# Kernel tuning notes

Measured on AMD Instinct MI355X. Metric: run time of the kernel, lower is better.

Reference implementation:

```python
import jax, jax.numpy as jnp
import numpy as np

D_MODEL = 512; D_INNER = 1024; D_STATE = 16; DT_RANK = 32; D_CONV = 4
N_LAYERS = 2; LSPP = 7; N_ROI = 2048; HIDDEN = 4096


def layer_norm(x, g, b, eps=1e-5):
    mu = x.mean(-1, keepdims=True)
    v = ((x - mu) ** 2).mean(-1, keepdims=True)
    return (x - mu) * jax.lax.rsqrt(v + eps) * g + b


def causal_dwconv(u, w, b):
    # u: [N,L,Di], w: [Di,K] depthwise, causal left-pad K-1
    x = jnp.transpose(u, (0, 2, 1))
    out = jax.lax.conv_general_dilated(x, w[:, None, :], (1,), [(D_CONV - 1, 0)],
                                       dimension_numbers=('NCH', 'OIH', 'NCH'),
                                       feature_group_count=D_INNER)
    return jnp.transpose(out, (0, 2, 1)) + b


def selective_scan(u, dt, A, B, C):
    # u, dt: [N,L,Di]; B, C: [N,L,S]; A: [Di,S]
    def step(h, xs):
        dt_t, B_t, C_t, u_t = xs
        dA = jnp.exp(dt_t[..., None] * A)                      # [N,Di,S]
        h = dA * h + (dt_t * u_t)[..., None] * B_t[:, None, :]
        return h, jnp.einsum('nds,ns->nd', h, C_t)
    h0 = jnp.zeros((u.shape[0], D_INNER, D_STATE), u.dtype)
    xs = (jnp.moveaxis(dt, 1, 0), jnp.moveaxis(B, 1, 0),
          jnp.moveaxis(C, 1, 0), jnp.moveaxis(u, 1, 0))
    _, ys = jax.lax.scan(step, h0, xs)
    return jnp.moveaxis(ys, 0, 1)                              # [N,L,Di]


def mamba_block(h, inw, cw, cb, xpw, dtw, dtb, Alog, Dp, ow):
    # decomposed bidirectional mamba ('dbm'): shared in_proj/gate, fwd+bwd scans summed
    xz = h @ inw.T                                             # [N,L,2*Di]
    xi, z = jnp.split(xz, 2, axis=-1)
    ys = []
    for d in range(2):
        u = xi if d == 0 else jnp.flip(xi, axis=1)
        u = jax.nn.silu(causal_dwconv(u, cw[d], cb[d]))
        dbl = u @ xpw[d].T                                     # [N,L,DT_RANK+2S]
        dtr = dbl[..., :DT_RANK]
        B = dbl[..., DT_RANK:DT_RANK + D_STATE]
        C = dbl[..., DT_RANK + D_STATE:]
        dt = jax.nn.softplus(dtr @ dtw[d].T + dtb[d])
        A = -jnp.exp(Alog[d])
        yd = selective_scan(u, dt, A, B, C) + u * Dp[d]
        ys.append(yd if d == 0 else jnp.flip(yd, axis=1))
    return ((ys[0] + ys[1]) * jax.nn.silu(z)) @ ow.T


def setup_inputs() -> dict:
    key = jax.random.key(0)
    ks = iter(jax.random.split(key, 40))
    rn = lambda shape, scale: jax.random.normal(next(ks), shape, dtype=jnp.float32) * scale
    inp = {}
    inp['x_flat'] = rn((N_ROI, D_MODEL * LSPP), 1.0)
    inp['conv_a_w'] = rn((256, 512, 3), (512 * 3) ** -0.5)
    inp['conv_p_w'] = rn((256, 512, 1), 512 ** -0.5)
    inp['se_w1'] = rn((32, 512), 512 ** -0.5)
    inp['se_b1'] = jnp.zeros((32,), jnp.float32)
    inp['se_w2'] = rn((512, 32), 32 ** -0.5)
    inp['se_b2'] = jnp.zeros((512,), jnp.float32)
    inp['ln_g'] = jnp.ones((N_LAYERS, D_MODEL), jnp.float32)
    inp['ln_b'] = jnp.zeros((N_LAYERS, D_MODEL), jnp.float32)
    inp['in_proj_w'] = rn((N_LAYERS, 2 * D_INNER, D_MODEL), D_MODEL ** -0.5)
    inp['conv_w'] = rn((N_LAYERS, 2, D_INNER, D_CONV), D_CONV ** -0.5)
    inp['conv_b'] = jnp.zeros((N_LAYERS, 2, D_INNER), jnp.float32)
    inp['x_proj_w'] = rn((N_LAYERS, 2, DT_RANK + 2 * D_STATE, D_INNER), D_INNER ** -0.5)
    inp['dt_proj_w'] = rn((N_LAYERS, 2, D_INNER, DT_RANK), DT_RANK ** -0.5)
    inp['dt_proj_b'] = rn((N_LAYERS, 2, D_INNER), 0.1) - 4.0
    inp['A_log'] = jnp.log(jnp.arange(1., D_STATE + 1., dtype=jnp.float32)) * jnp.ones((N_LAYERS, 2, D_INNER, D_STATE), jnp.float32)
    inp['D_param'] = jnp.ones((N_LAYERS, 2, D_INNER), jnp.float32)
    inp['out_proj_w'] = rn((N_LAYERS, D_MODEL, D_INNER), D_INNER ** -0.5)
    inp['out_ln_g'] = jnp.ones((D_MODEL,), jnp.float32)
    inp['out_ln_b'] = jnp.zeros((D_MODEL,), jnp.float32)
    inp['mlp_w1'] = rn((HIDDEN, D_MODEL), D_MODEL ** -0.5)
    inp['mlp_b1'] = jnp.zeros((HIDDEN,), jnp.float32)
    inp['mlp_w2'] = rn((HIDDEN, HIDDEN), HIDDEN ** -0.5)
    inp['mlp_b2'] = jnp.zeros((HIDDEN,), jnp.float32)
    return inp


def reference(x_flat, conv_a_w, conv_p_w, se_w1, se_b1, se_w2, se_b2, ln_g, ln_b,
              in_proj_w, conv_w, conv_b, x_proj_w, dt_proj_w, dt_proj_b, A_log,
              D_param, out_proj_w, out_ln_g, out_ln_b, mlp_w1, mlp_b1, mlp_w2, mlp_b2):
    N = x_flat.shape[0]
    x = x_flat.reshape(N, D_MODEL, LSPP)                       # [N,512,7]
    dn = ('NCH', 'OIH', 'NCH')
    # TSSE: strided conv branch + maxpool branch, concat, SE gating; L: 7 -> 4
    a = jax.nn.relu(jax.lax.conv_general_dilated(x, conv_a_w, (2,), [(1, 1)], dimension_numbers=dn))
    p = jax.lax.reduce_window(x, -jnp.inf, jax.lax.max, (1, 1, 3), (1, 1, 2), ((0, 0), (0, 0), (1, 1)))
    p = jax.nn.relu(jax.lax.conv_general_dilated(p, conv_p_w, (1,), [(0, 0)], dimension_numbers=dn))
    y = jnp.concatenate([a, p], axis=1)                        # [N,512,4]
    s = jax.nn.sigmoid(jax.nn.relu(y.mean(-1) @ se_w1.T + se_b1) @ se_w2.T + se_b2)
    y = y * s[:, :, None]
    # Mamba backbone: 2 pre-norm residual DBM blocks (mask is all-ones -> no-op)
    h = jnp.transpose(y, (0, 2, 1))                            # [N,L,512]
    for l in range(N_LAYERS):
        h = h + mamba_block(layer_norm(h, ln_g[l], ln_b[l]), in_proj_w[l], conv_w[l],
                            conv_b[l], x_proj_w[l], dt_proj_w[l], dt_proj_b[l],
                            A_log[l], D_param[l], out_proj_w[l])
    h = layer_norm(h, out_ln_g, out_ln_b)
    feat = h.mean(1)                                           # mean pool over time
    z1 = jax.nn.relu(feat @ mlp_w1.T + mlp_b1)
    return jax.nn.relu(z1 @ mlp_w2.T + mlp_b2)                 # [N,4096]
```

## Files before the change

### kernel.cpp

```cpp
#include <hip/hip_runtime.h>
#include <hip/hip_bf16.h>

typedef __hip_bfloat16 bf16;
typedef __attribute__((ext_vector_type(8))) short s16x8;
typedef __attribute__((ext_vector_type(4))) float f32x4;

__device__ __forceinline__ float u2f(unsigned short u){
  union { unsigned int i; float f; } v; v.i = ((unsigned int)u) << 16; return v.f;
}
__device__ __forceinline__ float bfu(bf16 x){ return __bfloat162float(x); }
__device__ __forceinline__ bf16  f2b(float x){ return __float2bfloat16(x); }

__device__ __forceinline__ void gload16(const void* g, void* l){
  __builtin_amdgcn_global_load_lds(
      (const __attribute__((address_space(1))) void*)g,
      (__attribute__((address_space(3))) void*)l, 16, 0, 0);
}

__device__ __forceinline__ float block_sum256(float v, float* red){
  #pragma unroll
  for (int o = 32; o > 0; o >>= 1) v += __shfl_down(v, o, 64);
  int lane = threadIdx.x & 63, wid = threadIdx.x >> 6;
  if (lane == 0) red[wid] = v;
  __syncthreads();
  float r = red[0] + red[1] + red[2] + red[3];
  __syncthreads();
  return r;
}

__global__ __launch_bounds__(256) void f2b4_kernel(
    const float4* __restrict__ in, ushort4* __restrict__ out, int n4)
{
  int stride = gridDim.x * 256;
  for (int i = blockIdx.x*256 + threadIdx.x; i < n4; i += stride){
    float4 v = in[i];
    ushort4 o;
    o.x = __bfloat16_as_ushort(f2b(v.x));
    o.y = __bfloat16_as_ushort(f2b(v.y));
    o.z = __bfloat16_as_ushort(f2b(v.z));
    o.w = __bfloat16_as_ushort(f2b(v.w));
    out[i] = o;
  }
}

__global__ __launch_bounds__(256) void xpw_pad_kernel(
    const float* __restrict__ xpw, bf16* __restrict__ out)
{
  int idx = blockIdx.x*256 + threadIdx.x;
  if (idx >= 524288) return;
  int l = idx >> 18, rem = idx & 262143, row = rem >> 10, c = rem & 1023;
  int d = row >> 7, r = row & 127;
  float v = (r < 64) ? xpw[(((size_t)l*2 + d)*64 + r)*1024 + c] : 0.f;
  out[idx] = f2b(v);
}

__global__ __launch_bounds__(256) void wdt_pad_kernel(
    const float* __restrict__ dtw, bf16* __restrict__ out)
{
  int idx = blockIdx.x*256 + threadIdx.x;
  if (idx >= 262144) return;
  int ld = idx >> 16, rem = idx & 65535, r = rem >> 6, c = rem & 63;
  float v = (c < 32) ? dtw[((size_t)ld*1024 + r)*32 + c] : 0.f;
  out[idx] = f2b(v);
}

__global__ __launch_bounds__(256) void atab_kernel(
    const float* __restrict__ Alog, float* __restrict__ Atab)
{
  int i = blockIdx.x*256 + threadIdx.x;
  if (i < 65536) Atab[i] = -__expf(Alog[i]);
}

template<int ACT, int OMODE, bool HASBIAS>
__global__ __launch_bounds__(256) void mgemm_kernel(
    const bf16* __restrict__ A, const bf16* __restrict__ W,
    const float* __restrict__ bias, void* __restrict__ outp,
    int K, int ldo)
{
  __shared__ char lsA[16384];
  __shared__ char lsB[16384];
  const int tid = threadIdx.x;
  const int w = tid >> 6, l = tid & 63;
  const int nwg = gridDim.x * gridDim.y;
  const int lin = blockIdx.y * gridDim.x + blockIdx.x;
  const int cpx = nwg >> 3;
  const int swz = (lin & 7) * cpx + (lin >> 3);
  const int m0 = (swz % gridDim.x) * 128, n0 = (swz / gridDim.x) * 128;
  const int wr = w >> 1, wc = w & 1;
  const size_t ldb = (size_t)K * 2;
  const char* Ab = (const char*)A + (size_t)m0 * ldb;
  const char* Wb = (const char*)W + (size_t)n0 * ldb;

  const int srow = l >> 3;
  const int scb  = ((l & 7) ^ srow) << 4;
  const int fr = l & 15;
  const int fg = l >> 4;
  const int fsw = (fr & 7) << 4;

  f32x4 acc[4][4];
  #pragma unroll
  for (int m = 0; m < 4; ++m)
    #pragma unroll
    for (int n = 0; n < 4; ++n) acc[m][n] = (f32x4){0.f,0.f,0.f,0.f};

  const int nk = K >> 6;
  for (int kt = 0; kt < nk; ++kt){
    const char* As = Ab + (size_t)kt * 128;
    const char* Ws = Wb + (size_t)kt * 128;
    #pragma unroll
    for (int i = 0; i < 4; ++i){
      int row = (i*4 + w)*8 + srow;
      gload16(As + (size_t)row*ldb + scb, &lsA[(i*4 + w)*1024]);
    }
    #pragma unroll
    for (int i = 0; i < 4; ++i){
      int row = (i*4 + w)*8 + srow;
      gload16(Ws + (size_t)row*ldb + scb, &lsB[(i*4 + w)*1024]);
    }
    __syncthreads();

    s16x8 af[4][2], bfr[4][2];
    #pragma unroll
    for (int m = 0; m < 4; ++m){
      int row = wr*64 + m*16 + fr;
      af[m][0] = *(const s16x8*)&lsA[row*128 + (( 0 + fg*16) ^ fsw)];
      af[m][1] = *(const s16x8*)&lsA[row*128 + ((64 + fg*16) ^ fsw)];
    }
    #pragma unroll
    for (int n = 0; n < 4; ++n){
      int row = wc*64 + n*16 + fr;
      bfr[n][0] = *(const s16x8*)&lsB[row*128 + (( 0 + fg*16) ^ fsw)];
      bfr[n][1] = *(const s16x8*)&lsB[row*128 + ((64 + fg*16) ^ fsw)];
    }
    #pragma unroll
    for (int m = 0; m < 4; ++m)
      #pragma unroll
      for (int n = 0; n < 4; ++n){
        acc[m][n] = __builtin_amdgcn_mfma_f32_16x16x32_bf16(af[m][0], bfr[n][0], acc[m][n], 0, 0, 0);
        acc[m][n] = __builtin_amdgcn_mfma_f32_16x16x32_bf16(af[m][1], bfr[n][1], acc[m][n], 0, 0, 0);
      }
    __syncthreads();
  }

  const int orow0 = m0 + wr*64, ocol0 = n0 + wc*64;
  #pragma unroll
  for (int n = 0; n < 4; ++n){
    int col = ocol0 + n*16 + fr;
    float bv = HASBIAS ? bias[col] : 0.f;
    #pragma unroll
    for (int m = 0; m < 4; ++m){
      int rbase = orow0 + m*16 + fg*4;
      #pragma unroll
      for (int r = 0; r < 4; ++r){
        float v = acc[m][n][r] + bv;
        if (ACT == 1) v = fmaxf(v, 0.f);
        if (ACT == 2) v = (v > 20.f) ? v : log1pf(__expf(v));
        size_t oi = (size_t)(rbase + r) * ldo + col;
        if (OMODE == 0)      ((bf16*)outp)[oi] = f2b(v);
        else if (OMODE == 1) ((float*)outp)[oi] = v;
        else                 ((float*)outp)[oi] += v;
      }
    }
  }
}

__global__ __launch_bounds__(256) void bgemm_kernel(
    const bf16* __restrict__ A, const bf16* __restrict__ W,
    bf16* __restrict__ dtr_buf, float* __restrict__ dbl)
{
  __shared__ char lsA[16384];
  __shared__ char lsB[16384];
  const int tid = threadIdx.x;
  const int w = tid >> 6, l = tid & 63;
  const int nwg = gridDim.x * 2;
  const int lin = blockIdx.y * gridDim.x + blockIdx.x;
  const int cpx = nwg >> 3;
  const int swz = (lin & 7) * cpx + (lin >> 3);
  const int m0 = (swz % gridDim.x) * 128;
  const int d  = swz / gridDim.x;
  const int K = 1024;
  const int wr = w >> 1, wc = w & 1;
  const size_t ldb = (size_t)K * 2;
  const char* Ab = (const char*)(A + (size_t)d*8388608) + (size_t)m0 * ldb;
  const char* Wb = (const char*)(W + (size_t)d*131072);

  const int srow = l >> 3;
  const int scb  = ((l & 7) ^ srow) << 4;
  const int fr = l & 15;
  const int fg = l >> 4;
  const int fsw = (fr & 7) << 4;

  f32x4 acc[4][4];
  #pragma unroll
  for (int m = 0; m < 4; ++m)
    #pragma unroll
    for (int n = 0; n < 4; ++n) acc[m][n] = (f32x4){0.f,0.f,0.f,0.f};

  const int nk = K >> 6;
  for (int kt = 0; kt < nk; ++kt){
    const char* As = Ab + (size_t)kt * 128;
    const char* Ws = Wb + (size_t)kt * 128;
    #pragma unroll
    for (int i = 0; i < 4; ++i){
      int row = (i*4 + w)*8 + srow;
      gload16(As + (size_t)row*ldb + scb, &lsA[(i*4 + w)*1024]);
    }
    #pragma unroll
    for (int i = 0; i < 4; ++i){
      int row = (i*4 + w)*8 + srow;
      gload16(Ws + (size_t)row*ldb + scb, &lsB[(i*4 + w)*1024]);
    }
    __syncthreads();

    s16x8 af[4][2], bfr[4][2];
    #pragma unroll
    for (int m = 0; m < 4; ++m){
      int row = wr*64 + m*16 + fr;
      af[m][0] = *(const s16x8*)&lsA[row*128 + (( 0 + fg*16) ^ fsw)];
      af[m][1] = *(const s16x8*)&lsA[row*128 + ((64 + fg*16) ^ fsw)];
    }
    #pragma unroll
    for (int n = 0; n < 4; ++n){
      int row = wc*64 + n*16 + fr;
      bfr[n][0] = *(const s16x8*)&lsB[row*128 + (( 0 + fg*16) ^ fsw)];
      bfr[n][1] = *(const s16x8*)&lsB[row*128 + ((64 + fg*16) ^ fsw)];
    }
    #pragma unroll
    for (int m = 0; m < 4; ++m)
      #pragma unroll
      for (int n = 0; n < 4; ++n){
        acc[m][n] = __builtin_amdgcn_mfma_f32_16x16x32_bf16(af[m][0], bfr[n][0], acc[m][n], 0, 0, 0);
        acc[m][n] = __builtin_amdgcn_mfma_f32_16x16x32_bf16(af[m][1], bfr[n][1], acc[m][n], 0, 0, 0);
      }
    __syncthreads();
  }

  const int orow0 = m0 + wr*64, c0 = wc*64;
  #pragma unroll
  for (int n = 0; n < 4; ++n){
    int col = c0 + n*16 + fr;
    #pragma unroll
    for (int m = 0; m < 4; ++m){
      int rbase = orow0 + m*16 + fg*4;
      #pragma unroll
      for (int r = 0; r < 4; ++r){
        float v = acc[m][n][r];
        int row = rbase + r;
        if (col < 32)
          dtr_buf[((size_t)d*8192 + row)*64 + col] = f2b(v);
        else if (col < 64)
          dbl[(size_t)row*128 + d*64 + (col - 32)] = v;
        else if (col < 96)
          dtr_buf[((size_t)d*8192 + row)*64 + (col - 32)] = f2b(v);
      }
    }
  }
}

__global__ __launch_bounds__(256) void im2col_kernel(
    const float* __restrict__ x_flat, bf16* __restrict__ Aa, bf16* __restrict__ P)
{
  __shared__ float xs[512][8];
  const int n = blockIdx.x, tid = threadIdx.x;
  const float* xr = x_flat + (size_t)n * 3584;
  for (int i = tid; i < 3584; i += 256) xs[i / 7][i % 7] = xr[i];
  __syncthreads();
  bf16* Ar = Aa + (size_t)n * 4 * 1536;
  for (int i = tid; i < 6144; i += 256){
    int t = i / 1536, col = i - t*1536;
    int c = col / 3, kk = col - c*3;
    int p = 2*t - 1 + kk;
    float v = (p >= 0 && p < 7) ? xs[c][p] : 0.f;
    Ar[i] = f2b(v);
  }
  bf16* Pr = P + (size_t)n * 4 * 512;
  for (int i = tid; i < 2048; i += 256){
    int t = i >> 9, c = i & 511;
    int st = 2*t - 1;
    float m = -1e30f;
    #pragma unroll
    for (int k = 0; k < 3; ++k){ int p = st + k; if (p >= 0 && p < 7) m = fmaxf(m, xs[c][p]); }
    Pr[i] = f2b(m);
  }
}

__global__ __launch_bounds__(256) void se_kernel(
    const float* __restrict__ sw1, const float* __restrict__ sb1,
    const float* __restrict__ sw2, const float* __restrict__ sb2,
    float* __restrict__ h)
{
  __shared__ float yms[512];
  __shared__ float s1s[32];
  const int n = blockIdx.x, tid = threadIdx.x;
  float* hb = h + (size_t)n * 2048;
  for (int c = tid; c < 512; c += 256)
    yms[c] = 0.25f * (hb[c] + hb[512+c] + hb[1024+c] + hb[1536+c]);
  __syncthreads();
  {
    int o = tid >> 3, sl = tid & 7;
    const float* wr = sw1 + (size_t)o * 512 + sl*64;
    const float* ym = yms + sl*64;
    float a = 0.f;
    #pragma unroll 16
    for (int i = 0; i < 64; ++i) a += wr[i] * ym[i];
    a += __shfl_down(a, 4, 8);
    a += __shfl_down(a, 2, 8);
    a += __shfl_down(a, 1, 8);
    if (sl == 0) s1s[o] = fmaxf(a + sb1[o], 0.f);
  }
  __syncthreads();
  for (int c = tid; c < 512; c += 256){
    float a = sb2[c];
    const float* wr = sw2 + (size_t)c * 32;
    #pragma unroll
    for (int j = 0; j < 32; ++j) a += wr[j] * s1s[j];
    float s = 1.f / (1.f + __expf(-a));
    #pragma unroll
    for (int t = 0; t < 4; ++t) hb[t*512 + c] *= s;
  }
}

__global__ __launch_bounds__(256) void ln_kernel(
    const float* __restrict__ x, const float* __restrict__ g,
    const float* __restrict__ b, bf16* __restrict__ out)
{
  __shared__ float red[4];
  const int row = blockIdx.x, t = threadIdx.x;
  const float* xr = x + (size_t)row * 512;
  float v0 = xr[t], v1 = xr[t + 256];
  float s = block_sum256(v0 + v1, red);
  float mu = s * (1.f/512.f);
  float d0 = v0 - mu, d1 = v1 - mu;
  float sq = block_sum256(d0*d0 + d1*d1, red);
  float rstd = rsqrtf(sq * (1.f/512.f) + 1e-5f);
  out[(size_t)row*512 + t]       = f2b(d0*rstd*g[t]     + b[t]);
  out[(size_t)row*512 + t + 256] = f2b(d1*rstd*g[t+256] + b[t+256]);
}

__global__ __launch_bounds__(256) void finalln_kernel(
    const float* __restrict__ h, const float* __restrict__ g,
    const float* __restrict__ b, bf16* __restrict__ feat)
{
  __shared__ float red[4];
  const int n = blockIdx.x, t = threadIdx.x;
  float a0 = 0.f, a1 = 0.f;
  for (int tt = 0; tt < 4; ++tt){
    const float* xr = h + ((size_t)n*4 + tt)*512;
    float v0 = xr[t], v1 = xr[t+256];
    float s = block_sum256(v0 + v1, red);
    float mu = s * (1.f/512.f);
    float d0 = v0 - mu, d1 = v1 - mu;
    float sq = block_sum256(d0*d0 + d1*d1, red);
    float rstd = rsqrtf(sq * (1.f/512.f) + 1e-5f);
    a0 += d0*rstd*g[t]     + b[t];
    a1 += d1*rstd*g[t+256] + b[t+256];
  }
  feat[(size_t)n*512 + t]       = f2b(a0 * 0.25f);
  feat[(size_t)n*512 + t + 256] = f2b(a1 * 0.25f);
}

__global__ __launch_bounds__(256) void dwconv2_kernel(
    const bf16* __restrict__ xz, const float* __restrict__ cw,
    const float* __restrict__ cb, bf16* __restrict__ u)
{
  const int n = blockIdx.x;
  const int c4 = threadIdx.x * 4;
  ushort4 in4[4];
  #pragma unroll
  for (int t = 0; t < 4; ++t)
    in4[t] = *reinterpret_cast<const ushort4*>(&xz[((size_t)n*4 + t)*2048 + c4]);
  #pragma unroll
  for (int d = 0; d < 2; ++d){
    const float* cwd = cw + d*4096;
    const float* cbd = cb + d*1024;
    ushort4 out[4];
    #pragma unroll
    for (int j = 0; j < 4; ++j){
      float xa[4];
      #pragma unroll
      for (int t = 0; t < 4; ++t){
        int ts = d ? 3 - t : t;
        unsigned short us = j==0?in4[ts].x : j==1?in4[ts].y : j==2?in4[ts].z : in4[ts].w;
        xa[t] = u2f(us);
      }
      float4 wv = *reinterpret_cast<const float4*>(&cwd[(c4 + j)*4]);
      float bb = cbd[c4 + j];
      float o[4];
      o[0] = xa[0]*wv.w + bb;
      o[1] = xa[0]*wv.z + xa[1]*wv.w + bb;
      o[2] = xa[0]*wv.y + xa[1]*wv.z + xa[2]*wv.w + bb;
      o[3] = xa[0]*wv.x + xa[1]*wv.y + xa[2]*wv.z + xa[3]*wv.w + bb;
      #pragma unroll
      for (int t = 0; t < 4; ++t){
        float v = o[t];
        float sv = v / (1.f + __expf(-v));
        unsigned short us = __bfloat16_as_ushort(f2b(sv));
        if (j==0) out[t].x = us; else if (j==1) out[t].y = us;
        else if (j==2) out[t].z = us; else out[t].w = us;
      }
    }
    #pragma unroll
    for (int t = 0; t < 4; ++t)
      *reinterpret_cast<ushort4*>(&u[(size_t)d*8388608 + ((size_t)n*4 + t)*1024 + c4]) = out[t];
  }
}

__global__ __launch_bounds__(256) void scan_kernel(
    const float* __restrict__ dbl, const bf16* __restrict__ dt,
    const bf16* __restrict__ ud, const float* __restrict__ Atab,
    const float* __restrict__ Dp, int d, bf16* __restrict__ yd)
{
  __shared__ float Bs[4][16], Cs[4][16];
  const int n = blockIdx.x, g = blockIdx.y, tid = threadIdx.x;
  if (tid < 128){
    int t = tid >> 5, j = tid & 31;
    float v = dbl[((size_t)n*4 + t)*128 + d*64 + j];
    if (j < 16) Bs[t][j] = v; else Cs[t][j-16] = v;
  }
  __syncthreads();
  const int c = g*256 + tid;
  float A[16];
  {
    const float4* ap = reinterpret_cast<const float4*>(Atab + (size_t)c*16);
    #pragma unroll
    for (int q = 0; q < 4; ++q){
      float4 v = ap[q];
      A[q*4+0] = v.x; A[q*4+1] = v.y; A[q*4+2] = v.z; A[q*4+3] = v.w;
    }
  }
  const float Dpc = Dp[c];
  float hs[16];
  #pragma unroll
  for (int s = 0; s < 16; ++s) hs[s] = 0.f;
  #pragma unroll
  for (int t = 0; t < 4; ++t){
    float dtv = bfu(dt[((size_t)n*4 + t)*1024 + c]);
    float uv  = bfu(ud[((size_t)n*4 + t)*1024 + c]);
    float du = dtv * uv;
    float yv = 0.f;
    #pragma unroll
    for (int s = 0; s < 16; ++s){
      float dA = __expf(dtv * A[s]);
      hs[s] = dA * hs[s] + du * Bs[t][s];
      yv += hs[s] * Cs[t][s];
    }
    float out = yv + uv * Dpc;
    int to = d ? (3 - t) : t;
    yd[((size_t)n*4 + to)*1024 + c] = f2b(out);
  }
}

__global__ __launch_bounds__(256) void gate_kernel(
    const bf16* __restrict__ y, const bf16* __restrict__ xz,
    bf16* __restrict__ gated)
{
  const int total4 = 8192 * 256;
  for (int i = blockIdx.x*256 + threadIdx.x; i < total4; i += 2048*256){
    int row = i >> 8, c4 = (i & 255) << 2;
    ushort4 a4 = reinterpret_cast<const ushort4*>(y)[i];
    ushort4 b4 = reinterpret_cast<const ushort4*>(y + 8388608)[i];
    ushort4 z4 = *reinterpret_cast<const ushort4*>(&xz[(size_t)row*2048 + 1024 + c4]);
    float y0 = u2f(a4.x) + u2f(b4.x), y1 = u2f(a4.y) + u2f(b4.y);
    float y2 = u2f(a4.z) + u2f(b4.z), y3 = u2f(a4.w) + u2f(b4.w);
    float z0 = u2f(z4.x), z1 = u2f(z4.y), z2 = u2f(z4.z), z3 = u2f(z4.w);
    ushort4 o;
    o.x = __bfloat16_as_ushort(f2b(y0 * z0 / (1.f + __expf(-z0))));
    o.y = __bfloat16_as_ushort(f2b(y1 * z1 / (1.f + __expf(-z1))));
    o.z = __bfloat16_as_ushort(f2b(y2 * z2 / (1.f + __expf(-z2))));
    o.w = __bfloat16_as_ushort(f2b(y3 * z3 / (1.f + __expf(-z3))));
    reinterpret_cast<ushort4*>(gated)[i] = o;
  }
}

extern "C" void kernel_launch(void* const* d_in, const int* in_sizes, int n_in,
                              void* d_out, int out_size, void* d_ws, size_t ws_size,
                              hipStream_t stream)
{
  const float* x_flat    = (const float*)d_in[0];
  const float* conv_a_w  = (const float*)d_in[1];
  const float* conv_p_w  = (const float*)d_in[2];
  const float* se_w1     = (const float*)d_in[3];
  const float* se_b1     = (const float*)d_in[4];
  const float* se_w2     = (const float*)d_in[5];
  const float* se_b2     = (const float*)d_in[6];
  const float* ln_g      = (const float*)d_in[7];
  const float* ln_b      = (const float*)d_in[8];
  const float* in_proj_w = (const float*)d_in[9];
  const float* conv_w    = (const float*)d_in[10];
  const float* conv_b    = (const float*)d_in[11];
  const float* x_proj_w  = (const float*)d_in[12];
  const float* dt_proj_w = (const float*)d_in[13];
  const float* dt_proj_b = (const float*)d_in[14];
  const float* A_log     = (const float*)d_in[15];
  const float* D_param   = (const float*)d_in[16];
  const float* out_proj_w= (const float*)d_in[17];
  const float* out_ln_g  = (const float*)d_in[18];
  const float* out_ln_b  = (const float*)d_in[19];
  const float* mlp_w1    = (const float*)d_in[20];
  const float* mlp_b1    = (const float*)d_in[21];
  const float* mlp_w2    = (const float*)d_in[22];
  const float* mlp_b2    = (const float*)d_in[23];

  char* ws = (char*)d_ws;
  const size_t OFF_H    = 0;
  const size_t OFF_HN   = OFF_H    + 16777216;
  const size_t OFF_XZ   = OFF_HN   + 8388608;
  const size_t OFF_U    = OFF_XZ   + 33554432;
  const size_t OFF_SCR  = OFF_U    + 33554432;
  const size_t OFF_YB   = OFF_SCR  + 25165824;
  const size_t OFF_WB   = OFF_YB   + 33554432;
  const size_t OFF_WXP  = OFF_WB   + 6291456;
  const size_t OFF_WDT  = OFF_WXP  + 1048576;
  const size_t OFF_ATAB = OFF_WDT  + 524288;

  float* h    = (float*)(ws + OFF_H);
  bf16*  hn   = (bf16*) (ws + OFF_HN);
  bf16*  xz   = (bf16*) (ws + OFF_XZ);
  bf16*  u    = (bf16*) (ws + OFF_U);
  float* dbl  = (float*)(ws + OFF_SCR);
  bf16*  dtrb = (bf16*) (ws + OFF_SCR + 4194304);
  bf16*  dtb_ = (bf16*) (ws + OFF_SCR + 6291456);
  bf16*  y    = (bf16*) (ws + OFF_YB);
  bf16*  feat = (bf16*) (ws + OFF_HN);
  bf16*  z1   = (bf16*) (ws + OFF_XZ);
  bf16*  wbi  = (bf16*) (ws + OFF_WB);
  bf16*  wbo  = (bf16*) (ws + OFF_WB + 4194304);
  bf16*  wxp  = (bf16*) (ws + OFF_WXP);
  bf16*  wdtp = (bf16*) (ws + OFF_WDT);
  float* Atab = (float*)(ws + OFF_ATAB);
  bf16*  wb1  = (bf16*) (ws + OFF_SCR);
  bf16*  wb2  = (bf16*) (ws + OFF_YB);
  bf16*  Aa   = (bf16*) (ws + OFF_SCR);
  bf16*  Pm   = (bf16*) (ws + OFF_YB);
  bf16*  wa   = (bf16*) (ws + OFF_YB + 8388608);
  bf16*  wp   = (bf16*) (ws + OFF_YB + 8388608 + 786432);
  float* outf = (float*)d_out;

  f2b4_kernel<<<512,  256, 0, stream>>>((const float4*)conv_a_w,   (ushort4*)wa,  98304);
  f2b4_kernel<<<256,  256, 0, stream>>>((const float4*)conv_p_w,   (ushort4*)wp,  32768);
  f2b4_kernel<<<2048, 256, 0, stream>>>((const float4*)in_proj_w,  (ushort4*)wbi, 524288);
  f2b4_kernel<<<1024, 256, 0, stream>>>((const float4*)out_proj_w, (ushort4*)wbo, 262144);
  xpw_pad_kernel<<<2048, 256, 0, stream>>>(x_proj_w, wxp);
  wdt_pad_kernel<<<1024, 256, 0, stream>>>(dt_proj_w, wdtp);
  atab_kernel<<<256, 256, 0, stream>>>(A_log, Atab);

  im2col_kernel<<<2048, 256, 0, stream>>>(x_flat, Aa, Pm);
  mgemm_kernel<1,1,false><<<dim3(64,2), 256, 0, stream>>>(
      Aa, wa, nullptr, h, 1536, 512);
  mgemm_kernel<1,1,false><<<dim3(64,2), 256, 0, stream>>>(
      Pm, wp, nullptr, (float*)h + 256, 512, 512);
  se_kernel<<<2048, 256, 0, stream>>>(se_w1, se_b1, se_w2, se_b2, h);

  for (int l = 0; l < 2; ++l){
    ln_kernel<<<8192, 256, 0, stream>>>(h, ln_g + l*512, ln_b + l*512, hn);
    mgemm_kernel<0,0,false><<<dim3(64,16), 256, 0, stream>>>(
        hn, wbi + (size_t)l*2048*512, nullptr, xz, 512, 2048);
    dwconv2_kernel<<<2048, 256, 0, stream>>>(
        xz, conv_w + (size_t)l*8192, conv_b + (size_t)l*2048, u);
    bgemm_kernel<<<dim3(64,2), 256, 0, stream>>>(
        u, wxp + (size_t)l*262144, dtrb, dbl);
    for (int d = 0; d < 2; ++d){
      int ld = l*2 + d;
      mgemm_kernel<2,0,true><<<dim3(64,8), 256, 0, stream>>>(
          dtrb + (size_t)d*8192*64, wdtp + (size_t)ld*65536,
          dt_proj_b + (size_t)ld*1024, dtb_, 64, 1024);
      scan_kernel<<<dim3(2048,4), 256, 0, stream>>>(
          dbl, dtb_, u + (size_t)d*8388608, Atab + (size_t)ld*16384,
          D_param + (size_t)ld*1024, d, y + (size_t)d*8388608);
    }
    gate_kernel<<<2048, 256, 0, stream>>>(y, xz, u );
    mgemm_kernel<0,2,false><<<dim3(64,4), 256, 0, stream>>>(
        u, wbo + (size_t)l*512*1024, nullptr, h, 1024, 512);
  }

  finalln_kernel<<<2048, 256, 0, stream>>>(h, out_ln_g, out_ln_b, feat);

  f2b4_kernel<<<1024, 256, 0, stream>>>((const float4*)mlp_w1, (ushort4*)wb1, 524288);
  f2b4_kernel<<<2048, 256, 0, stream>>>((const float4*)mlp_w2, (ushort4*)wb2, 4194304);

  mgemm_kernel<1,0,true><<<dim3(16,32), 256, 0, stream>>>(
      feat, wb1, mlp_b1, z1, 512, 4096);
  mgemm_kernel<1,1,true><<<dim3(16,32), 256, 0, stream>>>(
      z1, wb2, mlp_b2, outf, 4096, 4096);
}
```

Baseline: 738.5 us.

## Fuse forward/backward scans with SiLU gating into one kernel using exp2

Merges the two per-direction scan launches and the separate gate kernel into a single scan2 kernel. Each thread computes both directional scans for its channel, sums them, applies the SiLU(z) gate and writes the gated output directly. This removes the intermediate y buffer write/read and two launches per layer. The A table is also pre-scaled by log2(e) so the inner loop can use the hardware exp2 instruction. The output is written in place over u, which is safe only because each thread reads its u elements before writing them.

```diff
diff --git a/kernel.cpp b/kernel.cpp
--- a/kernel.cpp
+++ b/kernel.cpp
@@ -68,7 +68,7 @@
     const float* __restrict__ Alog, float* __restrict__ Atab)
 {
   int i = blockIdx.x*256 + threadIdx.x;
-  if (i < 65536) Atab[i] = -__expf(Alog[i]);
+  if (i < 65536) Atab[i] = -__expf(Alog[i]) * 1.44269504088896f;
 }
 
 template<int ACT, int OMODE, bool HASBIAS>
@@ -405,70 +405,82 @@
   }
 }
 
-__global__ __launch_bounds__(256) void scan_kernel(
-    const float* __restrict__ dbl, const bf16* __restrict__ dt,
-    const bf16* __restrict__ ud, const float* __restrict__ Atab,
-    const float* __restrict__ Dp, int d, bf16* __restrict__ yd)
-{
-  __shared__ float Bs[4][16], Cs[4][16];
+__global__ __launch_bounds__(256) void scan2_kernel(
+    const float* __restrict__ dbl, const bf16* __restrict__ dt2,
+    const bf16* __restrict__ u, const bf16* __restrict__ xz,
+    const float* __restrict__ Atab2, const float* __restrict__ Dp,
+    bf16* __restrict__ gated)
+{
+  __shared__ float Bs[2][4][16], Cs[2][4][16];
   const int n = blockIdx.x, g = blockIdx.y, tid = threadIdx.x;
-  if (tid < 128){
-    int t = tid >> 5, j = tid & 31;
-    float v = dbl[((size_t)n*4 + t)*128 + d*64 + j];
-    if (j < 16) Bs[t][j] = v; else Cs[t][j-16] = v;
+  {
+    int t = tid >> 6, j = tid & 63;
+    int d = j >> 5, jj = j & 31;
+    float v = dbl[((size_t)n*4 + t)*128 + d*64 + jj];
+    if (jj < 16) Bs[d][t][jj] = v; else Cs[d][t][jj-16] = v;
   }
   __syncthreads();
   const int c = g*256 + tid;
-  float A[16];
+  const size_t base = (size_t)n*4*1024 + c;
+  float yo0[4], yo1[4];
+  float hs[16];
   {
-    const float4* ap = reinterpret_cast<const float4*>(Atab + (size_t)c*16);
+    float A[16];
+    const float4* ap = reinterpret_cast<const float4*>(Atab2 + (size_t)c*16);
     #pragma unroll
     for (int q = 0; q < 4; ++q){
       float4 v = ap[q];
-      A[q*4+0] = v.x; A[q*4+1] = v.y; A[q*4+2] = v.z; A[q*4+3] = v.w;
-    }
-  }
-  const float Dpc = Dp[c];
-  float hs[16];
-  #pragma unroll
-  for (int s = 0; s < 16; ++s) hs[s] = 0.f;
+      A[q*4+0]=v.x; A[q*4+1]=v.y; A[q*4+2]=v.z; A[q*4+3]=v.w;
+    }
+    const float Dpc = Dp[c];
+    #pragma unroll
+    for (int s = 0; s < 16; ++s) hs[s] = 0.f;
+    #pragma unroll
+    for (int t = 0; t < 4; ++t){
+      float dtv = bfu(dt2[base + (size_t)t*1024]);
+      float uv  = bfu(u  [base + (size_t)t*1024]);
+      float du = dtv * uv;
+      float yv = 0.f;
+      #pragma unroll
+      for (int s = 0; s < 16; ++s){
+        float dA = __builtin_amdgcn_exp2f(dtv * A[s]);
+        hs[s] = dA * hs[s] + du * Bs[0][t][s];
+        yv += hs[s] * Cs[0][t][s];
+      }
+      yo0[t] = yv + uv * Dpc;
+    }
+  }
+  {
+    float A[16];
+    const float4* ap = reinterpret_cast<const float4*>(Atab2 + 16384 + (size_t)c*16);
+    #pragma unroll
+    for (int q = 0; q < 4; ++q){
+      float4 v = ap[q];
+      A[q*4+0]=v.x; A[q*4+1]=v.y; A[q*4+2]=v.z; A[q*4+3]=v.w;
+    }
+    const float Dpc = Dp[1024 + c];
+    #pragma unroll
+    for (int s = 0; s < 16; ++s) hs[s] = 0.f;
+    #pragma unroll
+    for (int t = 0; t < 4; ++t){
+      float dtv = bfu(dt2[8388608 + base + (size_t)t*1024]);
+      float uv  = bfu(u  [8388608 + base + (size_t)t*1024]);
+      float du = dtv * uv;
+      float yv = 0.f;
+      #pragma unroll
+      for (int s = 0; s < 16; ++s){
+        float dA = __builtin_amdgcn_exp2f(dtv * A[s]);
+        hs[s] = dA * hs[s] + du * Bs[1][t][s];
+        yv += hs[s] * Cs[1][t][s];
+      }
+      yo1[3 - t] = yv + uv * Dpc;
+    }
+  }
   #pragma unroll
   for (int t = 0; t < 4; ++t){
-    float dtv = bfu(dt[((size_t)n*4 + t)*1024 + c]);
-    float uv  = bfu(ud[((size_t)n*4 + t)*1024 + c]);
-    float du = dtv * uv;
-    float yv = 0.f;
-    #pragma unroll
-    for (int s = 0; s < 16; ++s){
-      float dA = __expf(dtv * A[s]);
-      hs[s] = dA * hs[s] + du * Bs[t][s];
-      yv += hs[s] * Cs[t][s];
-    }
-    float out = yv + uv * Dpc;
-    int to = d ? (3 - t) : t;
-    yd[((size_t)n*4 + to)*1024 + c] = f2b(out);
-  }
-}
-
-__global__ __launch_bounds__(256) void gate_kernel(
-    const bf16* __restrict__ y, const bf16* __restrict__ xz,
-    bf16* __restrict__ gated)
-{
-  const int total4 = 8192 * 256;
-  for (int i = blockIdx.x*256 + threadIdx.x; i < total4; i += 2048*256){
-    int row = i >> 8, c4 = (i & 255) << 2;
-    ushort4 a4 = reinterpret_cast<const ushort4*>(y)[i];
-    ushort4 b4 = reinterpret_cast<const ushort4*>(y + 8388608)[i];
-    ushort4 z4 = *reinterpret_cast<const ushort4*>(&xz[(size_t)row*2048 + 1024 + c4]);
-    float y0 = u2f(a4.x) + u2f(b4.x), y1 = u2f(a4.y) + u2f(b4.y);
-    float y2 = u2f(a4.z) + u2f(b4.z), y3 = u2f(a4.w) + u2f(b4.w);
-    float z0 = u2f(z4.x), z1 = u2f(z4.y), z2 = u2f(z4.z), z3 = u2f(z4.w);
-    ushort4 o;
-    o.x = __bfloat16_as_ushort(f2b(y0 * z0 / (1.f + __expf(-z0))));
-    o.y = __bfloat16_as_ushort(f2b(y1 * z1 / (1.f + __expf(-z1))));
-    o.z = __bfloat16_as_ushort(f2b(y2 * z2 / (1.f + __expf(-z2))));
-    o.w = __bfloat16_as_ushort(f2b(y3 * z3 / (1.f + __expf(-z3))));
-    reinterpret_cast<ushort4*>(gated)[i] = o;
+    float z = bfu(xz[(size_t)(n*4 + t)*2048 + 1024 + c]);
+    float sv = z / (1.f + __expf(-z));
+    gated[base + (size_t)t*1024] = f2b((yo0[t] + yo1[t]) * sv);
   }
 }
 
@@ -519,8 +531,7 @@
   bf16*  u    = (bf16*) (ws + OFF_U);
   float* dbl  = (float*)(ws + OFF_SCR);
   bf16*  dtrb = (bf16*) (ws + OFF_SCR + 4194304);
-  bf16*  dtb_ = (bf16*) (ws + OFF_SCR + 6291456);
-  bf16*  y    = (bf16*) (ws + OFF_YB);
+  bf16*  dt2  = (bf16*) (ws + OFF_YB);
   bf16*  feat = (bf16*) (ws + OFF_HN);
   bf16*  z1   = (bf16*) (ws + OFF_XZ);
   bf16*  wbi  = (bf16*) (ws + OFF_WB);
@@ -563,12 +574,11 @@
       int ld = l*2 + d;
       mgemm_kernel<2,0,true><<<dim3(64,8), 256, 0, stream>>>(
           dtrb + (size_t)d*8192*64, wdtp + (size_t)ld*65536,
-          dt_proj_b + (size_t)ld*1024, dtb_, 64, 1024);
-      scan_kernel<<<dim3(2048,4), 256, 0, stream>>>(
-          dbl, dtb_, u + (size_t)d*8388608, Atab + (size_t)ld*16384,
-          D_param + (size_t)ld*1024, d, y + (size_t)d*8388608);
-    }
-    gate_kernel<<<2048, 256, 0, stream>>>(y, xz, u );
+          dt_proj_b + (size_t)ld*1024, dt2 + (size_t)d*8388608, 64, 1024);
+    }
+    scan2_kernel<<<dim3(2048,4), 256, 0, stream>>>(
+        dbl, dt2, u, xz, Atab + (size_t)l*32768, D_param + (size_t)l*2048,
+        u );
     mgemm_kernel<0,2,false><<<dim3(64,4), 256, 0, stream>>>(
         u, wbo + (size_t)l*512*1024, nullptr, h, 1024, 512);
   }
```

After: 717.1 us. 1.03x faster.
